# Kernel tuning notes

Measured on AMD Instinct MI355X. Metric: run time of the kernel, lower is better.

## Reference

```python
import jax, jax.numpy as jnp
import numpy as np

B, S, D = 4, 4096, 1024
H, DH = 16, 64            # heads, head dim (D = H*DH)
W = 256                   # local window size; S % W == 0
HID = 2 * D               # GEGLU hidden dim
LN_EPS = 1e-5


def setup_inputs() -> dict:
    key = jax.random.key(0)
    ks = jax.random.split(key, 8)
    w = lambda k, shp: (jax.random.normal(k, shp, jnp.float32) * 0.02)
    return {
        "x": jax.random.normal(ks[0], (B, S, D), jnp.float32),
        "ln1_g": jnp.ones((D,), jnp.float32), "ln1_b": jnp.zeros((D,), jnp.float32),
        "ln2_g": jnp.ones((D,), jnp.float32), "ln2_b": jnp.zeros((D,), jnp.float32),
        "Wq": w(ks[1], (D, D)), "Wk": w(ks[2], (D, D)), "Wv": w(ks[3], (D, D)),
        "Wo": w(ks[4], (D, D)), "bo": jnp.zeros((D,), jnp.float32),
        "W1": w(ks[5], (D, 2 * HID)), "b1": jnp.zeros((2 * HID,), jnp.float32),
        "W2": w(ks[6], (HID, D)), "b2": jnp.zeros((D,), jnp.float32),
    }


def layer_norm(x, g, b):
    mu = jnp.mean(x, axis=-1, keepdims=True)
    var = jnp.mean(jnp.square(x - mu), axis=-1, keepdims=True)
    return (x - mu) * jax.lax.rsqrt(var + LN_EPS) * g + b


def local_causal_attention(x, Wq, Wk, Wv, Wo, bo):
    b, s, d = x.shape
    nw = s // W
    def split_heads(t):  # [b,s,d] -> [b,H,nw,W,DH]
        return t.reshape(b, s, H, DH).transpose(0, 2, 1, 3).reshape(b, H, nw, W, DH)
    q = split_heads(x @ Wq)
    k = split_heads(x @ Wk)
    v = split_heads(x @ Wv)
    # look_backward=1: each window attends to [prev window, current window]
    def with_prev(t):  # [b,H,nw,W,DH] -> [b,H,nw,2W,DH]
        prev = jnp.pad(t, ((0, 0), (0, 0), (1, 0), (0, 0), (0, 0)))[:, :, :-1]
        return jnp.concatenate([prev, t], axis=3)
    kc, vc = with_prev(k), with_prev(v)
    scores = jnp.einsum("bhnqd,bhnkd->bhnqk", q, kc) * (DH ** -0.5)
    # positions: qpos = n*W + i ; kpos = (n-1)*W + j, j in [0,2W)
    n = jnp.arange(nw)[:, None, None]
    i = jnp.arange(W)[None, :, None]
    j = jnp.arange(2 * W)[None, None, :]
    qpos = n * W + i
    kpos = (n - 1) * W + j
    mask = (kpos <= qpos) & (kpos >= 0)  # causal + left-edge padding
    scores = jnp.where(mask[None, None], scores, jnp.finfo(scores.dtype).min)
    attn = jax.nn.softmax(scores, axis=-1)
    out = jnp.einsum("bhnqk,bhnkd->bhnqd", attn, vc)
    out = out.reshape(b, H, s, DH).transpose(0, 2, 1, 3).reshape(b, s, d)
    return out @ Wo + bo


def geglu(x, W1, b1, W2, b2):
    h = x @ W1 + b1
    a, g = jnp.split(h, 2, axis=-1)
    return (a * jax.nn.gelu(g, approximate=False)) @ W2 + b2


def reference(x, ln1_g, ln1_b, ln2_g, ln2_b, Wq, Wk, Wv, Wo, bo, W1, b1, W2, b2):
    x = x + local_causal_attention(layer_norm(x, ln1_g, ln1_b), Wq, Wk, Wv, Wo, bo)
    x = x + geglu(layer_norm(x, ln2_g, ln2_b), W1, b1, W2, b2)
    return x
```

## Files before the change

kernel.cpp:

```cpp
#include <hip/hip_runtime.h>
#include <hip/hip_bf16.h>

typedef __attribute__((ext_vector_type(4))) float f32x4;
typedef __attribute__((ext_vector_type(8))) short bf16x8;
typedef __attribute__((ext_vector_type(8))) unsigned short u16x8;

static __device__ __forceinline__ ushort f2b(float f) {
  union { float f; unsigned u; } v; v.f = f;
  unsigned r = v.u + 0x7fffu + ((v.u >> 16) & 1u);
  return (ushort)(r >> 16);
}

static __device__ __forceinline__ float gelu_fast(float g) {
  const float c0 = 0.7978845608028654f, c1 = 0.044715f;
  const float u = c0 * (g + c1 * g * g * g);
  const float e = __expf(2.0f * u);
  const float t = 1.0f - 2.0f / (e + 1.0f);
  return 0.5f * g * (1.0f + t);
}

static __device__ __forceinline__ void gload_lds16(const void* g, void* l) {
  __builtin_amdgcn_global_load_lds(
      (__attribute__((address_space(1))) void*)(g),
      (__attribute__((address_space(3))) void*)(l), 16, 0, 0);
}

__global__ __launch_bounds__(256) void transpose_cast_kernel(
    const float* __restrict__ W, ushort* __restrict__ Wt, int K, int N) {
  __shared__ float tile[32][33];
  const int n0 = blockIdx.x * 32, k0 = blockIdx.y * 32;
  const int tx = threadIdx.x, ty = threadIdx.y;
#pragma unroll
  for (int r = 0; r < 32; r += 8)
    tile[ty + r][tx] = W[(size_t)(k0 + ty + r) * N + n0 + tx];
  __syncthreads();
#pragma unroll
  for (int r = 0; r < 32; r += 8)
    Wt[(size_t)(n0 + ty + r) * K + k0 + tx] = f2b(tile[tx][ty + r]);
}

__global__ __launch_bounds__(256) void ln_kernel(
    const float* __restrict__ x, const float* __restrict__ g,
    const float* __restrict__ bb, ushort* __restrict__ out) {
  const int row = blockIdx.x;
  const float* xr = x + (size_t)row * 1024;
  const float4 v = *(const float4*)&xr[threadIdx.x * 4];
  float s = v.x + v.y + v.z + v.w;
  float s2 = v.x * v.x + v.y * v.y + v.z * v.z + v.w * v.w;
#pragma unroll
  for (int off = 32; off > 0; off >>= 1) {
    s += __shfl_down(s, off);
    s2 += __shfl_down(s2, off);
  }
  __shared__ float red[8];
  const int lane = threadIdx.x & 63, wv = threadIdx.x >> 6;
  if (lane == 0) { red[wv] = s; red[4 + wv] = s2; }
  __syncthreads();
  s = red[0] + red[1] + red[2] + red[3];
  s2 = red[4] + red[5] + red[6] + red[7];
  const float mu = s * (1.0f / 1024.0f);
  const float rs = rsqrtf(s2 * (1.0f / 1024.0f) - mu * mu + 1e-5f);
  const int c = threadIdx.x * 4;
  ushort4 o;
  o.x = f2b((v.x - mu) * rs * g[c + 0] + bb[c + 0]);
  o.y = f2b((v.y - mu) * rs * g[c + 1] + bb[c + 1]);
  o.z = f2b((v.z - mu) * rs * g[c + 2] + bb[c + 2]);
  o.w = f2b((v.w - mu) * rs * g[c + 3] + bb[c + 3]);
  *(ushort4*)&out[(size_t)row * 1024 + c] = o;
}

template <int MODE>
__global__ __launch_bounds__(512) void gemm256_kernel(
    const ushort* __restrict__ A, const ushort* __restrict__ Bt,
    const int M, const int N, const int K,
    ushort* __restrict__ Cb, float* __restrict__ Cf,
    const float* __restrict__ bias, const float* __restrict__ res) {
  __shared__ __align__(16) ushort lds[3 * 16384];

  const int ntn = N >> 8;
  const int bn = blockIdx.x % ntn;
  const int bm = blockIdx.x / ntn;
  const int tid = threadIdx.x;
  const int l = tid & 63, w = tid >> 6;
  const int wm = w >> 2, wn = w & 3;
  const int fr = l & 15, fq = l >> 4;

  const ushort* Ab = A + (size_t)bm * 256 * K;
  const ushort* Bb = Bt + (size_t)bn * 256 * K;

  const int srow = (l >> 2);
  const int scol = (((l & 3) ^ ((l >> 3) & 3)) * 8);

  f32x4 acc[8][4];
#pragma unroll
  for (int m = 0; m < 8; m++)
#pragma unroll
    for (int n = 0; n < 4; n++) acc[m][n] = (f32x4)0.0f;

  const int NT = K >> 5;

#define STAGE256(t)                                                            \
  {                                                                            \
    const int b3 = (t) % 3;                                                    \
    const size_t kk = (size_t)(t) * 32;                                        \
    _Pragma("unroll") for (int i = 0; i < 2; i++) {                            \
      const int r = (w * 2 + i) * 16 + srow;                                   \
      gload_lds16(Ab + (size_t)r * K + kk + scol,                              \
                  &lds[b3 * 16384 + (w * 2 + i) * 512]);                       \
      gload_lds16(Bb + (size_t)r * K + kk + scol,                              \
                  &lds[b3 * 16384 + 8192 + (w * 2 + i) * 512]);                \
    }                                                                          \
  }

  STAGE256(0);
  STAGE256(1);

  for (int t = 0; t < NT; ++t) {
    if (t + 2 < NT) {
      STAGE256(t + 2);
      asm volatile("s_waitcnt vmcnt(8)" ::: "memory");
    } else if (t + 1 < NT) {
      asm volatile("s_waitcnt vmcnt(4)" ::: "memory");
    } else {
      asm volatile("s_waitcnt vmcnt(0)" ::: "memory");
    }
    __builtin_amdgcn_s_barrier();
    asm volatile("" ::: "memory");

    const ushort* La = &lds[(t % 3) * 16384];
    const ushort* Lb = La + 8192;

    bf16x8 af[8], bf[4];
#pragma unroll
    for (int m = 0; m < 8; m++) {
      const int r = wm * 128 + m * 16 + fr;
      af[m] = *(const bf16x8*)&La[r * 32 + ((fq ^ ((r >> 1) & 3)) * 8)];
    }
#pragma unroll
    for (int n = 0; n < 4; n++) {
      const int r = wn * 64 + n * 16 + fr;
      bf[n] = *(const bf16x8*)&Lb[r * 32 + ((fq ^ ((r >> 1) & 3)) * 8)];
    }

    __builtin_amdgcn_s_setprio(1);
#pragma unroll
    for (int m = 0; m < 8; m++)
#pragma unroll
      for (int n = 0; n < 4; n++)
        acc[m][n] = __builtin_amdgcn_mfma_f32_16x16x32_bf16(af[m], bf[n], acc[m][n], 0, 0, 0);
    __builtin_amdgcn_s_setprio(0);

    asm volatile("" ::: "memory");
    __builtin_amdgcn_s_barrier();
  }
#undef STAGE256

  const int rowb = bm * 256 + wm * 128 + fq * 4;
  const int colb = bn * 256 + wn * 64 + fr;
#pragma unroll
  for (int m = 0; m < 8; m++) {
#pragma unroll
    for (int n = 0; n < 4; n++) {
      const int col = colb + n * 16;
#pragma unroll
      for (int j = 0; j < 4; j++) {
        const int row = rowb + m * 16 + j;
        float vv = acc[m][n][j];
        if (MODE == 0) {
          Cb[(size_t)row * N + col] = f2b(vv);
        } else if (MODE == 2) {
          if (col < 1024) vv *= 0.125f;
          Cb[(size_t)row * N + col] = f2b(vv);
        } else {
          Cf[(size_t)row * N + col] = vv + bias[col] + res[(size_t)row * N + col];
        }
      }
    }
  }
}

__global__ __launch_bounds__(512) void gemm_geglu_kernel(
    const ushort* __restrict__ A, const ushort* __restrict__ W1t,
    const float* __restrict__ b1, ushort* __restrict__ U) {
  const int K = 1024;
  __shared__ __align__(16) ushort lds[3 * 16384];

  const int bn = blockIdx.x & 15;
  const int bm = blockIdx.x >> 4;
  const int tid = threadIdx.x;
  const int l = tid & 63, w = tid >> 6;
  const int wm = w >> 2, wn = w & 3;
  const int fr = l & 15, fq = l >> 4;

  const ushort* Ab = A + (size_t)bm * 256 * K;
  const ushort* Bab = W1t + (size_t)bn * 128 * K;
  const ushort* Bgb = W1t + (size_t)(2048 + bn * 128) * K;

  const int srow = (l >> 2);
  const int scol = (((l & 3) ^ ((l >> 3) & 3)) * 8);
  const int brow = (tid >> 2);
  const int bscol = (((tid & 3) ^ ((tid >> 3) & 3)) * 8);

  f32x4 acca[8][2], accg[8][2];
#pragma unroll
  for (int m = 0; m < 8; m++)
#pragma unroll
    for (int n = 0; n < 2; n++) { acca[m][n] = (f32x4)0.0f; accg[m][n] = (f32x4)0.0f; }

  const int NT = K >> 5;

#define STAGEGL(t)                                                             \
  {                                                                            \
    const int b3 = (t) % 3;                                                    \
    const size_t kk = (size_t)(t) * 32;                                        \
    _Pragma("unroll") for (int i = 0; i < 2; i++) {                            \
      const int r = (w * 2 + i) * 16 + srow;                                   \
      gload_lds16(Ab + (size_t)r * K + kk + scol,                              \
                  &lds[b3 * 16384 + (w * 2 + i) * 512]);                       \
    }                                                                          \
    gload_lds16(Bab + (size_t)brow * K + kk + bscol,                           \
                &lds[b3 * 16384 + 8192 + w * 512]);                            \
    gload_lds16(Bgb + (size_t)brow * K + kk + bscol,                           \
                &lds[b3 * 16384 + 12288 + w * 512]);                           \
  }

  STAGEGL(0);
  STAGEGL(1);

  for (int t = 0; t < NT; ++t) {
    if (t + 2 < NT) {
      STAGEGL(t + 2);
      asm volatile("s_waitcnt vmcnt(8)" ::: "memory");
    } else if (t + 1 < NT) {
      asm volatile("s_waitcnt vmcnt(4)" ::: "memory");
    } else {
      asm volatile("s_waitcnt vmcnt(0)" ::: "memory");
    }
    __builtin_amdgcn_s_barrier();
    asm volatile("" ::: "memory");

    const ushort* La = &lds[(t % 3) * 16384];
    const ushort* Lba = La + 8192;
    const ushort* Lbg = La + 12288;

    bf16x8 af[8], ba[2], bg[2];
#pragma unroll
    for (int m = 0; m < 8; m++) {
      const int r = wm * 128 + m * 16 + fr;
      af[m] = *(const bf16x8*)&La[r * 32 + ((fq ^ ((r >> 1) & 3)) * 8)];
    }
#pragma unroll
    for (int n = 0; n < 2; n++) {
      const int r = wn * 32 + n * 16 + fr;
      ba[n] = *(const bf16x8*)&Lba[r * 32 + ((fq ^ ((r >> 1) & 3)) * 8)];
      bg[n] = *(const bf16x8*)&Lbg[r * 32 + ((fq ^ ((r >> 1) & 3)) * 8)];
    }

    __builtin_amdgcn_s_setprio(1);
#pragma unroll
    for (int m = 0; m < 8; m++)
#pragma unroll
      for (int n = 0; n < 2; n++) {
        acca[m][n] = __builtin_amdgcn_mfma_f32_16x16x32_bf16(af[m], ba[n], acca[m][n], 0, 0, 0);
        accg[m][n] = __builtin_amdgcn_mfma_f32_16x16x32_bf16(af[m], bg[n], accg[m][n], 0, 0, 0);
      }
    __builtin_amdgcn_s_setprio(0);

    asm volatile("" ::: "memory");
    __builtin_amdgcn_s_barrier();
  }
#undef STAGEGL

  const int rowb = bm * 256 + wm * 128 + fq * 4;
  const int colb = bn * 128 + wn * 32 + fr;
#pragma unroll
  for (int m = 0; m < 8; m++) {
#pragma unroll
    for (int n = 0; n < 2; n++) {
      const int col = colb + n * 16;
      const float b1a = b1[col];
      const float b1g = b1[2048 + col];
#pragma unroll
      for (int j = 0; j < 4; j++) {
        const int row = rowb + m * 16 + j;
        const float a = acca[m][n][j] + b1a;
        const float gg = accg[m][n][j] + b1g;
        U[(size_t)row * 2048 + col] = f2b(a * gelu_fast(gg));
      }
    }
  }
}

__global__ __launch_bounds__(256, 3) void attn_kernel(
    const ushort* __restrict__ Q, const ushort* __restrict__ Kb,
    const ushort* __restrict__ Vb, ushort* __restrict__ O, const int qs) {
  const int bx = blockIdx.x;
  const int n = bx & 15;
  const int h = (bx >> 4) & 15;
  const int b = bx >> 8;
  const int tid = threadIdx.x;
  const int lane = tid & 63, wv = tid >> 6;
  const int fr = lane & 15, fq = lane >> 4;

  __shared__ __align__(16) ushort Kl[64 * 72];
  __shared__ __align__(16) ushort Vt[64 * 70];
  __shared__ __align__(16) ushort Pl[4][64 * 68];

  const size_t qrow0 = (size_t)b * 4096 + (size_t)n * 256;

  bf16x8 qf[4][2];
#pragma unroll
  for (int m = 0; m < 4; m++)
#pragma unroll
    for (int kh = 0; kh < 2; kh++)
      qf[m][kh] = *(const bf16x8*)&Q[(qrow0 + wv * 64 + m * 16 + fr) * qs + h * 64 + kh * 32 + fq * 8];

  f32x4 oacc[4][4];
#pragma unroll
  for (int m = 0; m < 4; m++)
#pragma unroll
    for (int d = 0; d < 4; d++) oacc[m][d] = (f32x4)0.0f;

  float lsum[4][4];
#pragma unroll
  for (int m = 0; m < 4; m++)
#pragma unroll
    for (int j = 0; j < 4; j++) lsum[m][j] = 0.0f;

  const int c0 = (n == 0) ? 4 : 0;
  for (int c = c0; c < 8; c++) {
    const size_t kvrow0 =
        (size_t)((long long)b * 4096 + (long long)n * 256 + (long long)c * 64 - 256);
#pragma unroll
    for (int p = 0; p < 2; p++) {
      const int s = tid + p * 256;
      const int rr = s >> 3, cs2 = s & 7;
      *(u16x8*)&Kl[rr * 72 + cs2 * 8] =
          *(const u16x8*)&Kb[(kvrow0 + rr) * qs + h * 64 + cs2 * 8];
      const u16x8 vvv = *(const u16x8*)&Vb[(kvrow0 + rr) * qs + h * 64 + cs2 * 8];
#pragma unroll
      for (int i = 0; i < 8; i++) Vt[(cs2 * 8 + i) * 70 + rr] = vvv[i];
    }
    __syncthreads();

    if (c <= wv + 4) {
      const bool diag = (c == wv + 4);
#pragma unroll
      for (int nn = 0; nn < 4; nn++) {
        f32x4 sa[4];
#pragma unroll
        for (int m = 0; m < 4; m++) sa[m] = (f32x4)0.0f;
#pragma unroll
        for (int kh = 0; kh < 2; kh++) {
          const bf16x8 bk = *(const bf16x8*)&Kl[(nn * 16 + fr) * 72 + kh * 32 + fq * 8];
#pragma unroll
          for (int m = 0; m < 4; m++)
            sa[m] = __builtin_amdgcn_mfma_f32_16x16x32_bf16(qf[m][kh], bk, sa[m], 0, 0, 0);
        }
#pragma unroll
        for (int m = 0; m < 4; m++)
#pragma unroll
          for (int j = 0; j < 4; j++) {
            float p = __expf(sa[m][j]);
            if (diag && (nn * 16 + fr > m * 16 + fq * 4 + j)) p = 0.0f;
            lsum[m][j] += p;
            Pl[wv][(m * 16 + fq * 4 + j) * 68 + nn * 16 + fr] = f2b(p);
          }
      }
      __builtin_amdgcn_s_setprio(1);
#pragma unroll
      for (int kh = 0; kh < 2; kh++) {
        bf16x8 pa[4];
#pragma unroll
        for (int m = 0; m < 4; m++)
          pa[m] = *(const bf16x8*)&Pl[wv][(m * 16 + fr) * 68 + kh * 32 + fq * 8];
#pragma unroll
        for (int d = 0; d < 4; d++) {
          const bf16x8 vb = *(const bf16x8*)&Vt[(d * 16 + fr) * 70 + kh * 32 + fq * 8];
#pragma unroll
          for (int m = 0; m < 4; m++)
            oacc[m][d] = __builtin_amdgcn_mfma_f32_16x16x32_bf16(pa[m], vb, oacc[m][d], 0, 0, 0);
        }
      }
      __builtin_amdgcn_s_setprio(0);
    }
    __syncthreads();
  }

  float rl[4][4];
#pragma unroll
  for (int m = 0; m < 4; m++)
#pragma unroll
    for (int j = 0; j < 4; j++) {
      float t = lsum[m][j];
      t += __shfl_xor(t, 1);
      t += __shfl_xor(t, 2);
      t += __shfl_xor(t, 4);
      t += __shfl_xor(t, 8);
      rl[m][j] = 1.0f / t;
    }

#pragma unroll
  for (int m = 0; m < 4; m++)
#pragma unroll
    for (int d = 0; d < 4; d++)
#pragma unroll
      for (int j = 0; j < 4; j++) {
        const float o = oacc[m][d][j] * rl[m][j];
        O[(qrow0 + wv * 64 + m * 16 + fq * 4 + j) * 1024 + h * 64 + d * 16 + fr] = f2b(o);
      }
}

extern "C" void kernel_launch(void* const* d_in, const int* in_sizes, int n_in,
                              void* d_out, int out_size, void* d_ws, size_t ws_size,
                              hipStream_t stream) {
  (void)in_sizes; (void)n_in; (void)out_size; (void)ws_size;
  const float* x     = (const float*)d_in[0];
  const float* ln1_g = (const float*)d_in[1];
  const float* ln1_b = (const float*)d_in[2];
  const float* ln2_g = (const float*)d_in[3];
  const float* ln2_b = (const float*)d_in[4];
  const float* Wq    = (const float*)d_in[5];
  const float* Wk    = (const float*)d_in[6];
  const float* Wv    = (const float*)d_in[7];
  const float* Wo    = (const float*)d_in[8];
  const float* bo    = (const float*)d_in[9];
  const float* W1    = (const float*)d_in[10];
  const float* b1    = (const float*)d_in[11];
  const float* W2    = (const float*)d_in[12];
  const float* b2    = (const float*)d_in[13];

  char* ws = (char*)d_ws;
  const size_t MB = 1ull << 20;
  ushort* WQKVT = (ushort*)(ws + 0 * MB);
  ushort* WOT = (ushort*)(ws + 6 * MB);
  ushort* W1T = (ushort*)(ws + 8 * MB);
  ushort* W2T = (ushort*)(ws + 16 * MB);
  ushort* LN1 = (ushort*)(ws + 20 * MB);
  ushort* ATT = LN1;
  ushort* QKV = (ushort*)(ws + 52 * MB);
  ushort* LN2 = (ushort*)(ws + 52 * MB);
  ushort* U   = (ushort*)(ws + 84 * MB);
  float*  X1  = (float*)d_out;
  float*  OUT = (float*)d_out;

  const dim3 tb(32, 8);
  transpose_cast_kernel<<<dim3(32, 32), tb, 0, stream>>>(Wq, WQKVT, 1024, 1024);
  transpose_cast_kernel<<<dim3(32, 32), tb, 0, stream>>>(Wk, WQKVT + (size_t)1024 * 1024, 1024, 1024);
  transpose_cast_kernel<<<dim3(32, 32), tb, 0, stream>>>(Wv, WQKVT + (size_t)2048 * 1024, 1024, 1024);
  transpose_cast_kernel<<<dim3(32, 32), tb, 0, stream>>>(Wo, WOT, 1024, 1024);
  transpose_cast_kernel<<<dim3(128, 32), tb, 0, stream>>>(W1, W1T, 1024, 4096);
  transpose_cast_kernel<<<dim3(32, 64), tb, 0, stream>>>(W2, W2T, 2048, 1024);

  ln_kernel<<<16384, 256, 0, stream>>>(x, ln1_g, ln1_b, LN1);

  gemm256_kernel<2><<<64 * 12, 512, 0, stream>>>(LN1, WQKVT, 16384, 3072, 1024,
                                                 QKV, nullptr, nullptr, nullptr);

  attn_kernel<<<1024, 256, 0, stream>>>(QKV, QKV + 1024, QKV + 2048, ATT, 3072);

  gemm256_kernel<1><<<64 * 4, 512, 0, stream>>>(ATT, WOT, 16384, 1024, 1024,
                                                nullptr, X1, bo, x);

  ln_kernel<<<16384, 256, 0, stream>>>(X1, ln2_g, ln2_b, LN2);

  gemm_geglu_kernel<<<64 * 16, 512, 0, stream>>>(LN2, W1T, b1, U);

  gemm256_kernel<1><<<64 * 4, 512, 0, stream>>>(U, W2T, 16384, 1024, 2048,
                                                nullptr, OUT, b2, X1);
}
```

Baseline: 557.0 us.

## Restructure GEMM mainloops to BK=64 double-buffered, four-phase interleaved loads

Both the 256x256 GEMM and the fused GEGLU GEMM move from a triple-buffered BK=32 pipeline to a double-buffered BK=64 pipeline with an 8-way XOR swizzle. Each K-step is split into four quarter-tile MFMA phases, and the next tile's global-to-LDS loads are spread across those phases. The aim is to halve loop iterations and barrier overhead per K and to overlap loads with compute at finer grain. In exchange there are more barriers per iteration, only one tile of prefetch depth, and LDS grows to 128KB, which limits occupancy.

```diff
diff --git a/kernel.cpp b/kernel.cpp
--- a/kernel.cpp
+++ b/kernel.cpp
@@ -24,6 +24,8 @@
       (__attribute__((address_space(1))) void*)(g),
       (__attribute__((address_space(3))) void*)(l), 16, 0, 0);
 }
+
+#define MFMA_BF16 __builtin_amdgcn_mfma_f32_16x16x32_bf16
 
 __global__ __launch_bounds__(256) void transpose_cast_kernel(
     const float* __restrict__ W, ushort* __restrict__ Wt, int K, int N) {
@@ -75,7 +77,7 @@
     const int M, const int N, const int K,
     ushort* __restrict__ Cb, float* __restrict__ Cf,
     const float* __restrict__ bias, const float* __restrict__ res) {
-  __shared__ __align__(16) ushort lds[3 * 16384];
+  __shared__ __align__(16) ushort lds[2 * 32768];
 
   const int ntn = N >> 8;
   const int bn = blockIdx.x % ntn;
@@ -88,8 +90,8 @@
   const ushort* Ab = A + (size_t)bm * 256 * K;
   const ushort* Bb = Bt + (size_t)bn * 256 * K;
 
-  const int srow = (l >> 2);
-  const int scol = (((l & 3) ^ ((l >> 3) & 3)) * 8);
+  const int lr = l >> 3;
+  const int sc = (((l & 7) ^ lr) * 8);
 
   f32x4 acc[8][4];
 #pragma unroll
@@ -97,63 +99,121 @@
 #pragma unroll
     for (int n = 0; n < 4; n++) acc[m][n] = (f32x4)0.0f;
 
-  const int NT = K >> 5;
-
-#define STAGE256(t)                                                            \
-  {                                                                            \
-    const int b3 = (t) % 3;                                                    \
-    const size_t kk = (size_t)(t) * 32;                                        \
-    _Pragma("unroll") for (int i = 0; i < 2; i++) {                            \
-      const int r = (w * 2 + i) * 16 + srow;                                   \
-      gload_lds16(Ab + (size_t)r * K + kk + scol,                              \
-                  &lds[b3 * 16384 + (w * 2 + i) * 512]);                       \
-      gload_lds16(Bb + (size_t)r * K + kk + scol,                              \
-                  &lds[b3 * 16384 + 8192 + (w * 2 + i) * 512]);                \
-    }                                                                          \
-  }
-
-  STAGE256(0);
-  STAGE256(1);
+  const int NT = K >> 6;
+
+#define STG_A(h, tt)                                                           \
+  { _Pragma("unroll") for (int i = 0; i < 2; i++) {                            \
+      const int rr = (h) * 128 + i * 64 + w * 8;                               \
+      gload_lds16(Ab + (size_t)(rr + lr) * K + (size_t)(tt) * 64 + sc,         \
+                  &lds[((tt) & 1) * 32768 + rr * 64]); } }
+#define STG_B(h, tt)                                                           \
+  { _Pragma("unroll") for (int i = 0; i < 2; i++) {                            \
+      const int rr = (h) * 128 + i * 64 + w * 8;                               \
+      gload_lds16(Bb + (size_t)(rr + lr) * K + (size_t)(tt) * 64 + sc,         \
+                  &lds[((tt) & 1) * 32768 + 16384 + rr * 64]); } }
+
+  STG_A(0, 0); STG_A(1, 0); STG_B(0, 0); STG_B(1, 0);
 
   for (int t = 0; t < NT; ++t) {
-    if (t + 2 < NT) {
-      STAGE256(t + 2);
-      asm volatile("s_waitcnt vmcnt(8)" ::: "memory");
-    } else if (t + 1 < NT) {
-      asm volatile("s_waitcnt vmcnt(4)" ::: "memory");
+    const ushort* La = &lds[(t & 1) * 32768];
+    const ushort* Lb = La + 16384;
+    bf16x8 af[4][2], bf[4][2];
+
+    if (t + 1 < NT) {
+      STG_A(0, t + 1);
+      asm volatile("s_waitcnt vmcnt(2)" ::: "memory");
     } else {
       asm volatile("s_waitcnt vmcnt(0)" ::: "memory");
     }
     __builtin_amdgcn_s_barrier();
     asm volatile("" ::: "memory");
-
-    const ushort* La = &lds[(t % 3) * 16384];
-    const ushort* Lb = La + 8192;
-
-    bf16x8 af[8], bf[4];
-#pragma unroll
-    for (int m = 0; m < 8; m++) {
+#pragma unroll
+    for (int m = 0; m < 4; m++) {
       const int r = wm * 128 + m * 16 + fr;
-      af[m] = *(const bf16x8*)&La[r * 32 + ((fq ^ ((r >> 1) & 3)) * 8)];
-    }
-#pragma unroll
-    for (int n = 0; n < 4; n++) {
+#pragma unroll
+      for (int kk = 0; kk < 2; kk++)
+        af[m][kk] = *(const bf16x8*)&La[r * 64 + (((kk * 4 + fq) ^ (r & 7)) * 8)];
+    }
+#pragma unroll
+    for (int n = 0; n < 2; n++) {
       const int r = wn * 64 + n * 16 + fr;
-      bf[n] = *(const bf16x8*)&Lb[r * 32 + ((fq ^ ((r >> 1) & 3)) * 8)];
-    }
-
-    __builtin_amdgcn_s_setprio(1);
-#pragma unroll
-    for (int m = 0; m < 8; m++)
-#pragma unroll
-      for (int n = 0; n < 4; n++)
-        acc[m][n] = __builtin_amdgcn_mfma_f32_16x16x32_bf16(af[m], bf[n], acc[m][n], 0, 0, 0);
-    __builtin_amdgcn_s_setprio(0);
-
+#pragma unroll
+      for (int kk = 0; kk < 2; kk++)
+        bf[n][kk] = *(const bf16x8*)&Lb[r * 64 + (((kk * 4 + fq) ^ (r & 7)) * 8)];
+    }
+    __builtin_amdgcn_s_setprio(1);
+#pragma unroll
+    for (int m = 0; m < 4; m++)
+#pragma unroll
+      for (int n = 0; n < 2; n++)
+#pragma unroll
+        for (int kk = 0; kk < 2; kk++)
+          acc[m][n] = MFMA_BF16(af[m][kk], bf[n][kk], acc[m][n], 0, 0, 0);
+    __builtin_amdgcn_s_setprio(0);
+    asm volatile("" ::: "memory");
+    __builtin_amdgcn_s_barrier();
+
+    if (t + 1 < NT) STG_A(1, t + 1);
+#pragma unroll
+    for (int n = 2; n < 4; n++) {
+      const int r = wn * 64 + n * 16 + fr;
+#pragma unroll
+      for (int kk = 0; kk < 2; kk++)
+        bf[n][kk] = *(const bf16x8*)&Lb[r * 64 + (((kk * 4 + fq) ^ (r & 7)) * 8)];
+    }
+    __builtin_amdgcn_s_barrier();
+    asm volatile("" ::: "memory");
+    __builtin_amdgcn_s_setprio(1);
+#pragma unroll
+    for (int m = 0; m < 4; m++)
+#pragma unroll
+      for (int n = 2; n < 4; n++)
+#pragma unroll
+        for (int kk = 0; kk < 2; kk++)
+          acc[m][n] = MFMA_BF16(af[m][kk], bf[n][kk], acc[m][n], 0, 0, 0);
+    __builtin_amdgcn_s_setprio(0);
+    asm volatile("" ::: "memory");
+    __builtin_amdgcn_s_barrier();
+
+    if (t + 1 < NT) STG_B(0, t + 1);
+#pragma unroll
+    for (int m = 0; m < 4; m++) {
+      const int r = wm * 128 + (m + 4) * 16 + fr;
+#pragma unroll
+      for (int kk = 0; kk < 2; kk++)
+        af[m][kk] = *(const bf16x8*)&La[r * 64 + (((kk * 4 + fq) ^ (r & 7)) * 8)];
+    }
+    __builtin_amdgcn_s_barrier();
+    asm volatile("" ::: "memory");
+    __builtin_amdgcn_s_setprio(1);
+#pragma unroll
+    for (int m = 0; m < 4; m++)
+#pragma unroll
+      for (int n = 0; n < 2; n++)
+#pragma unroll
+        for (int kk = 0; kk < 2; kk++)
+          acc[m + 4][n] = MFMA_BF16(af[m][kk], bf[n][kk], acc[m + 4][n], 0, 0, 0);
+    __builtin_amdgcn_s_setprio(0);
+    asm volatile("" ::: "memory");
+    __builtin_amdgcn_s_barrier();
+
+    if (t + 1 < NT) STG_B(1, t + 1);
+    __builtin_amdgcn_s_barrier();
+    asm volatile("" ::: "memory");
+    __builtin_amdgcn_s_setprio(1);
+#pragma unroll
+    for (int m = 0; m < 4; m++)
+#pragma unroll
+      for (int n = 2; n < 4; n++)
+#pragma unroll
+        for (int kk = 0; kk < 2; kk++)
+          acc[m + 4][n] = MFMA_BF16(af[m][kk], bf[n][kk], acc[m + 4][n], 0, 0, 0);
+    __builtin_amdgcn_s_setprio(0);
     asm volatile("" ::: "memory");
     __builtin_amdgcn_s_barrier();
   }
-#undef STAGE256
+#undef STG_A
+#undef STG_B
 
   const int rowb = bm * 256 + wm * 128 + fq * 4;
   const int colb = bn * 256 + wn * 64 + fr;
@@ -183,7 +243,7 @@
     const ushort* __restrict__ A, const ushort* __restrict__ W1t,
     const float* __restrict__ b1, ushort* __restrict__ U) {
   const int K = 1024;
-  __shared__ __align__(16) ushort lds[3 * 16384];
+  __shared__ __align__(16) ushort lds[2 * 32768];
 
   const int bn = blockIdx.x & 15;
   const int bm = blockIdx.x >> 4;
@@ -196,10 +256,8 @@
   const ushort* Bab = W1t + (size_t)bn * 128 * K;
   const ushort* Bgb = W1t + (size_t)(2048 + bn * 128) * K;
 
-  const int srow = (l >> 2);
-  const int scol = (((l & 3) ^ ((l >> 3) & 3)) * 8);
-  const int brow = (tid >> 2);
-  const int bscol = (((tid & 3) ^ ((tid >> 3) & 3)) * 8);
+  const int lr = l >> 3;
+  const int sc = (((l & 7) ^ lr) * 8);
 
   f32x4 acca[8][2], accg[8][2];
 #pragma unroll
@@ -207,69 +265,128 @@
 #pragma unroll
     for (int n = 0; n < 2; n++) { acca[m][n] = (f32x4)0.0f; accg[m][n] = (f32x4)0.0f; }
 
-  const int NT = K >> 5;
-
-#define STAGEGL(t)                                                             \
-  {                                                                            \
-    const int b3 = (t) % 3;                                                    \
-    const size_t kk = (size_t)(t) * 32;                                        \
-    _Pragma("unroll") for (int i = 0; i < 2; i++) {                            \
-      const int r = (w * 2 + i) * 16 + srow;                                   \
-      gload_lds16(Ab + (size_t)r * K + kk + scol,                              \
-                  &lds[b3 * 16384 + (w * 2 + i) * 512]);                       \
-    }                                                                          \
-    gload_lds16(Bab + (size_t)brow * K + kk + bscol,                           \
-                &lds[b3 * 16384 + 8192 + w * 512]);                            \
-    gload_lds16(Bgb + (size_t)brow * K + kk + bscol,                           \
-                &lds[b3 * 16384 + 12288 + w * 512]);                           \
-  }
-
-  STAGEGL(0);
-  STAGEGL(1);
+  const int NT = K >> 6;
+
+#define STG_GA(h, tt)                                                          \
+  { _Pragma("unroll") for (int i = 0; i < 2; i++) {                            \
+      const int rr = (h) * 128 + i * 64 + w * 8;                               \
+      gload_lds16(Ab + (size_t)(rr + lr) * K + (size_t)(tt) * 64 + sc,         \
+                  &lds[((tt) & 1) * 32768 + rr * 64]); } }
+#define STG_BA(tt)                                                             \
+  { _Pragma("unroll") for (int i = 0; i < 2; i++) {                            \
+      const int rr = i * 64 + w * 8;                                           \
+      gload_lds16(Bab + (size_t)(rr + lr) * K + (size_t)(tt) * 64 + sc,        \
+                  &lds[((tt) & 1) * 32768 + 16384 + rr * 64]); } }
+#define STG_BG(tt)                                                             \
+  { _Pragma("unroll") for (int i = 0; i < 2; i++) {                            \
+      const int rr = i * 64 + w * 8;                                           \
+      gload_lds16(Bgb + (size_t)(rr + lr) * K + (size_t)(tt) * 64 + sc,        \
+                  &lds[((tt) & 1) * 32768 + 24576 + rr * 64]); } }
+
+  STG_GA(0, 0); STG_GA(1, 0); STG_BA(0); STG_BG(0);
 
   for (int t = 0; t < NT; ++t) {
-    if (t + 2 < NT) {
-      STAGEGL(t + 2);
-      asm volatile("s_waitcnt vmcnt(8)" ::: "memory");
-    } else if (t + 1 < NT) {
-      asm volatile("s_waitcnt vmcnt(4)" ::: "memory");
+    const ushort* La = &lds[(t & 1) * 32768];
+    const ushort* Lba = La + 16384;
+    const ushort* Lbg = La + 24576;
+    bf16x8 af[4][2], ba[2][2], bg[2][2];
+
+    if (t + 1 < NT) {
+      STG_GA(0, t + 1);
+      asm volatile("s_waitcnt vmcnt(2)" ::: "memory");
     } else {
       asm volatile("s_waitcnt vmcnt(0)" ::: "memory");
     }
     __builtin_amdgcn_s_barrier();
     asm volatile("" ::: "memory");
-
-    const ushort* La = &lds[(t % 3) * 16384];
-    const ushort* Lba = La + 8192;
-    const ushort* Lbg = La + 12288;
-
-    bf16x8 af[8], ba[2], bg[2];
-#pragma unroll
-    for (int m = 0; m < 8; m++) {
+#pragma unroll
+    for (int m = 0; m < 4; m++) {
       const int r = wm * 128 + m * 16 + fr;
-      af[m] = *(const bf16x8*)&La[r * 32 + ((fq ^ ((r >> 1) & 3)) * 8)];
+#pragma unroll
+      for (int kk = 0; kk < 2; kk++)
+        af[m][kk] = *(const bf16x8*)&La[r * 64 + (((kk * 4 + fq) ^ (r & 7)) * 8)];
     }
 #pragma unroll
     for (int n = 0; n < 2; n++) {
       const int r = wn * 32 + n * 16 + fr;
-      ba[n] = *(const bf16x8*)&Lba[r * 32 + ((fq ^ ((r >> 1) & 3)) * 8)];
-      bg[n] = *(const bf16x8*)&Lbg[r * 32 + ((fq ^ ((r >> 1) & 3)) * 8)];
-    }
-
-    __builtin_amdgcn_s_setprio(1);
-#pragma unroll
-    for (int m = 0; m < 8; m++)
-#pragma unroll
-      for (int n = 0; n < 2; n++) {
-        acca[m][n] = __builtin_amdgcn_mfma_f32_16x16x32_bf16(af[m], ba[n], acca[m][n], 0, 0, 0);
-        accg[m][n] = __builtin_amdgcn_mfma_f32_16x16x32_bf16(af[m], bg[n], accg[m][n], 0, 0, 0);
-      }
-    __builtin_amdgcn_s_setprio(0);
-
+#pragma unroll
+      for (int kk = 0; kk < 2; kk++)
+        ba[n][kk] = *(const bf16x8*)&Lba[r * 64 + (((kk * 4 + fq) ^ (r & 7)) * 8)];
+    }
+    __builtin_amdgcn_s_setprio(1);
+#pragma unroll
+    for (int m = 0; m < 4; m++)
+#pragma unroll
+      for (int n = 0; n < 2; n++)
+#pragma unroll
+        for (int kk = 0; kk < 2; kk++)
+          acca[m][n] = MFMA_BF16(af[m][kk], ba[n][kk], acca[m][n], 0, 0, 0);
+    __builtin_amdgcn_s_setprio(0);
+    asm volatile("" ::: "memory");
+    __builtin_amdgcn_s_barrier();
+
+    if (t + 1 < NT) STG_GA(1, t + 1);
+#pragma unroll
+    for (int n = 0; n < 2; n++) {
+      const int r = wn * 32 + n * 16 + fr;
+#pragma unroll
+      for (int kk = 0; kk < 2; kk++)
+        bg[n][kk] = *(const bf16x8*)&Lbg[r * 64 + (((kk * 4 + fq) ^ (r & 7)) * 8)];
+    }
+    __builtin_amdgcn_s_barrier();
+    asm volatile("" ::: "memory");
+    __builtin_amdgcn_s_setprio(1);
+#pragma unroll
+    for (int m = 0; m < 4; m++)
+#pragma unroll
+      for (int n = 0; n < 2; n++)
+#pragma unroll
+        for (int kk = 0; kk < 2; kk++)
+          accg[m][n] = MFMA_BF16(af[m][kk], bg[n][kk], accg[m][n], 0, 0, 0);
+    __builtin_amdgcn_s_setprio(0);
+    asm volatile("" ::: "memory");
+    __builtin_amdgcn_s_barrier();
+
+    if (t + 1 < NT) STG_BA(t + 1);
+#pragma unroll
+    for (int m = 0; m < 4; m++) {
+      const int r = wm * 128 + (m + 4) * 16 + fr;
+#pragma unroll
+      for (int kk = 0; kk < 2; kk++)
+        af[m][kk] = *(const bf16x8*)&La[r * 64 + (((kk * 4 + fq) ^ (r & 7)) * 8)];
+    }
+    __builtin_amdgcn_s_barrier();
+    asm volatile("" ::: "memory");
+    __builtin_amdgcn_s_setprio(1);
+#pragma unroll
+    for (int m = 0; m < 4; m++)
+#pragma unroll
+      for (int n = 0; n < 2; n++)
+#pragma unroll
+        for (int kk = 0; kk < 2; kk++)
+          acca[m + 4][n] = MFMA_BF16(af[m][kk], ba[n][kk], acca[m + 4][n], 0, 0, 0);
+    __builtin_amdgcn_s_setprio(0);
+    asm volatile("" ::: "memory");
+    __builtin_amdgcn_s_barrier();
+
+    if (t + 1 < NT) STG_BG(t + 1);
+    __builtin_amdgcn_s_barrier();
+    asm volatile("" ::: "memory");
+    __builtin_amdgcn_s_setprio(1);
+#pragma unroll
+    for (int m = 0; m < 4; m++)
+#pragma unroll
+      for (int n = 0; n < 2; n++)
+#pragma unroll
+        for (int kk = 0; kk < 2; kk++)
+          accg[m + 4][n] = MFMA_BF16(af[m][kk], bg[n][kk], accg[m + 4][n], 0, 0, 0);
+    __builtin_amdgcn_s_setprio(0);
     asm volatile("" ::: "memory");
     __builtin_amdgcn_s_barrier();
   }
-#undef STAGEGL
+#undef STG_GA
+#undef STG_BA
+#undef STG_BG
 
   const int rowb = bm * 256 + wm * 128 + fq * 4;
   const int colb = bn * 128 + wn * 32 + fr;
@@ -355,7 +472,7 @@
           const bf16x8 bk = *(const bf16x8*)&Kl[(nn * 16 + fr) * 72 + kh * 32 + fq * 8];
 #pragma unroll
           for (int m = 0; m < 4; m++)
-            sa[m] = __builtin_amdgcn_mfma_f32_16x16x32_bf16(qf[m][kh], bk, sa[m], 0, 0, 0);
+            sa[m] = MFMA_BF16(qf[m][kh], bk, sa[m], 0, 0, 0);
         }
 #pragma unroll
         for (int m = 0; m < 4; m++)
@@ -379,7 +496,7 @@
           const bf16x8 vb = *(const bf16x8*)&Vt[(d * 16 + fr) * 70 + kh * 32 + fq * 8];
 #pragma unroll
           for (int m = 0; m < 4; m++)
-            oacc[m][d] = __builtin_amdgcn_mfma_f32_16x16x32_bf16(pa[m], vb, oacc[m][d], 0, 0, 0);
+            oacc[m][d] = MFMA_BF16(pa[m], vb, oacc[m][d], 0, 0, 0);
         }
       }
       __builtin_amdgcn_s_setprio(0);
```

New measurement: 535.7 us. 3.8% less time.

## Restructure GEMM mainloops into K=64 double-buffered four-phase schedule with interleaved loads

Applied to the files above, without the earlier changes.

Both the generic 256x256 GEMM and the fused GEGLU GEMM move from a triple-buffered K=32 pipeline to a double-buffered K=64 tile. Each tile is split into four compute phases, and the next tile's global->LDS loads are issued in pieces between phases. The LDS layout gains a wider 8-way XOR swizzle, and launch bounds now request two blocks per CU. The goal is fewer barriers per unit of work and better overlap of loads with MFMA, at the cost of more barriers inside each tile and tighter register and LDS pressure.

```diff
diff --git a/kernel.cpp b/kernel.cpp
--- a/kernel.cpp
+++ b/kernel.cpp
@@ -24,6 +24,8 @@
       (__attribute__((address_space(1))) void*)(g),
       (__attribute__((address_space(3))) void*)(l), 16, 0, 0);
 }
+
+#define MFMA_BF16 __builtin_amdgcn_mfma_f32_16x16x32_bf16
 
 __global__ __launch_bounds__(256) void transpose_cast_kernel(
     const float* __restrict__ W, ushort* __restrict__ Wt, int K, int N) {
@@ -70,12 +72,12 @@
 }
 
 template <int MODE>
-__global__ __launch_bounds__(512) void gemm256_kernel(
+__global__ __launch_bounds__(512, 2) void gemm256_kernel(
     const ushort* __restrict__ A, const ushort* __restrict__ Bt,
     const int M, const int N, const int K,
     ushort* __restrict__ Cb, float* __restrict__ Cf,
     const float* __restrict__ bias, const float* __restrict__ res) {
-  __shared__ __align__(16) ushort lds[3 * 16384];
+  __shared__ __align__(16) ushort lds[2 * 32768];
 
   const int ntn = N >> 8;
   const int bn = blockIdx.x % ntn;
@@ -88,8 +90,19 @@
   const ushort* Ab = A + (size_t)bm * 256 * K;
   const ushort* Bb = Bt + (size_t)bn * 256 * K;
 
-  const int srow = (l >> 2);
-  const int scol = (((l & 3) ^ ((l >> 3) & 3)) * 8);
+  const int lr = l >> 3;
+  const int sc = (((l & 7) ^ lr) * 8);
+
+  const char* ldsc = (const char*)lds;
+  const int fr7 = fr & 7;
+  const unsigned s0 = (unsigned)((fq ^ fr7) * 16);
+  const unsigned s1 = (unsigned)(((4 + fq) ^ fr7) * 16);
+  const unsigned cA0 = (unsigned)((wm * 128 + fr) * 128) + s0;
+  const unsigned cA1 = (unsigned)((wm * 128 + fr) * 128) + s1;
+  const unsigned cB0 = 32768u + (unsigned)((wn * 64 + fr) * 128) + s0;
+  const unsigned cB1 = 32768u + (unsigned)((wn * 64 + fr) * 128) + s1;
+  const unsigned dA0 = cA0 + 65536u, dA1 = cA1 + 65536u;
+  const unsigned dB0 = cB0 + 65536u, dB1 = cB1 + 65536u;
 
   f32x4 acc[8][4];
 #pragma unroll
@@ -97,63 +110,102 @@
 #pragma unroll
     for (int n = 0; n < 4; n++) acc[m][n] = (f32x4)0.0f;
 
-  const int NT = K >> 5;
-
-#define STAGE256(t)                                                            \
+  const int NT = K >> 6;
+
+#define STG_A(h, tt, DSTU)                                                     \
+  { _Pragma("unroll") for (int i = 0; i < 2; i++) {                            \
+      const int rr = (h) * 128 + i * 64 + w * 8;                               \
+      gload_lds16(Ab + (size_t)(rr + lr) * K + (size_t)(tt) * 64 + sc,         \
+                  &lds[(DSTU) + rr * 64]); } }
+#define STG_B(h, tt, DSTU)                                                     \
+  { _Pragma("unroll") for (int i = 0; i < 2; i++) {                            \
+      const int rr = (h) * 128 + i * 64 + w * 8;                               \
+      gload_lds16(Bb + (size_t)(rr + lr) * K + (size_t)(tt) * 64 + sc,         \
+                  &lds[(DSTU) + 16384 + rr * 64]); } }
+
+#define GPHASES(tt, bA0v, bA1v, bB0v, bB1v, DSTU, HASNEXT)                     \
   {                                                                            \
-    const int b3 = (t) % 3;                                                    \
-    const size_t kk = (size_t)(t) * 32;                                        \
-    _Pragma("unroll") for (int i = 0; i < 2; i++) {                            \
-      const int r = (w * 2 + i) * 16 + srow;                                   \
-      gload_lds16(Ab + (size_t)r * K + kk + scol,                              \
-                  &lds[b3 * 16384 + (w * 2 + i) * 512]);                       \
-      gload_lds16(Bb + (size_t)r * K + kk + scol,                              \
-                  &lds[b3 * 16384 + 8192 + (w * 2 + i) * 512]);                \
-    }                                                                          \
-  }
-
-  STAGE256(0);
-  STAGE256(1);
-
-  for (int t = 0; t < NT; ++t) {
-    if (t + 2 < NT) {
-      STAGE256(t + 2);
-      asm volatile("s_waitcnt vmcnt(8)" ::: "memory");
-    } else if (t + 1 < NT) {
-      asm volatile("s_waitcnt vmcnt(4)" ::: "memory");
-    } else {
-      asm volatile("s_waitcnt vmcnt(0)" ::: "memory");
-    }
-    __builtin_amdgcn_s_barrier();
-    asm volatile("" ::: "memory");
-
-    const ushort* La = &lds[(t % 3) * 16384];
-    const ushort* Lb = La + 8192;
-
-    bf16x8 af[8], bf[4];
-#pragma unroll
-    for (int m = 0; m < 8; m++) {
-      const int r = wm * 128 + m * 16 + fr;
-      af[m] = *(const bf16x8*)&La[r * 32 + ((fq ^ ((r >> 1) & 3)) * 8)];
-    }
-#pragma unroll
-    for (int n = 0; n < 4; n++) {
-      const int r = wn * 64 + n * 16 + fr;
-      bf[n] = *(const bf16x8*)&Lb[r * 32 + ((fq ^ ((r >> 1) & 3)) * 8)];
-    }
-
-    __builtin_amdgcn_s_setprio(1);
-#pragma unroll
-    for (int m = 0; m < 8; m++)
-#pragma unroll
-      for (int n = 0; n < 4; n++)
-        acc[m][n] = __builtin_amdgcn_mfma_f32_16x16x32_bf16(af[m], bf[n], acc[m][n], 0, 0, 0);
-    __builtin_amdgcn_s_setprio(0);
-
-    asm volatile("" ::: "memory");
-    __builtin_amdgcn_s_barrier();
-  }
-#undef STAGE256
+    bf16x8 af[4][2], bfv[4][2];                                                \
+                                  \
+    if (HASNEXT) {                                                             \
+      STG_A(0, (tt) + 1, DSTU);                                                \
+      asm volatile("s_waitcnt vmcnt(2)" ::: "memory");                         \
+    } else {                                                                   \
+      asm volatile("s_waitcnt vmcnt(0)" ::: "memory");                         \
+    }                                                                          \
+    __builtin_amdgcn_s_barrier();                                              \
+    asm volatile("" ::: "memory");                                             \
+    _Pragma("unroll") for (int m = 0; m < 4; m++) {                            \
+      af[m][0] = *(const bf16x8*)(ldsc + (bA0v) + m * 2048);                   \
+      af[m][1] = *(const bf16x8*)(ldsc + (bA1v) + m * 2048);                   \
+    }                                                                          \
+    _Pragma("unroll") for (int n = 0; n < 2; n++) {                            \
+      bfv[n][0] = *(const bf16x8*)(ldsc + (bB0v) + n * 2048);                  \
+      bfv[n][1] = *(const bf16x8*)(ldsc + (bB1v) + n * 2048);                  \
+    }                                                                          \
+    __builtin_amdgcn_s_setprio(1);                                             \
+    _Pragma("unroll") for (int m = 0; m < 4; m++)                              \
+      _Pragma("unroll") for (int n = 0; n < 2; n++)                            \
+        _Pragma("unroll") for (int kk = 0; kk < 2; kk++)                       \
+          acc[m][n] = MFMA_BF16(af[m][kk], bfv[n][kk], acc[m][n], 0, 0, 0);    \
+    __builtin_amdgcn_s_setprio(0);                                             \
+    asm volatile("" ::: "memory");                                             \
+    __builtin_amdgcn_s_barrier();                                              \
+                                                \
+    if (HASNEXT) STG_A(1, (tt) + 1, DSTU);                                     \
+    _Pragma("unroll") for (int n = 2; n < 4; n++) {                            \
+      bfv[n][0] = *(const bf16x8*)(ldsc + (bB0v) + n * 2048);                  \
+      bfv[n][1] = *(const bf16x8*)(ldsc + (bB1v) + n * 2048);                  \
+    }                                                                          \
+    __builtin_amdgcn_s_barrier();                                              \
+    asm volatile("" ::: "memory");                                             \
+    __builtin_amdgcn_s_setprio(1);                                             \
+    _Pragma("unroll") for (int m = 0; m < 4; m++)                              \
+      _Pragma("unroll") for (int n = 2; n < 4; n++)                            \
+        _Pragma("unroll") for (int kk = 0; kk < 2; kk++)                       \
+          acc[m][n] = MFMA_BF16(af[m][kk], bfv[n][kk], acc[m][n], 0, 0, 0);    \
+    __builtin_amdgcn_s_setprio(0);                                             \
+    asm volatile("" ::: "memory");                                             \
+    __builtin_amdgcn_s_barrier();                                              \
+                                                \
+    if (HASNEXT) STG_B(0, (tt) + 1, DSTU);                                     \
+    _Pragma("unroll") for (int m = 0; m < 4; m++) {                            \
+      af[m][0] = *(const bf16x8*)(ldsc + (bA0v) + (m + 4) * 2048);             \
+      af[m][1] = *(const bf16x8*)(ldsc + (bA1v) + (m + 4) * 2048);             \
+    }                                                                          \
+    __builtin_amdgcn_s_barrier();                                              \
+    asm volatile("" ::: "memory");                                             \
+    __builtin_amdgcn_s_setprio(1);                                             \
+    _Pragma("unroll") for (int m = 0; m < 4; m++)                              \
+      _Pragma("unroll") for (int n = 0; n < 2; n++)                            \
+        _Pragma("unroll") for (int kk = 0; kk < 2; kk++)                       \
+          acc[m + 4][n] = MFMA_BF16(af[m][kk], bfv[n][kk], acc[m + 4][n], 0, 0, 0); \
+    __builtin_amdgcn_s_setprio(0);                                             \
+    asm volatile("" ::: "memory");                                             \
+    __builtin_amdgcn_s_barrier();                                              \
+                                                \
+    if (HASNEXT) STG_B(1, (tt) + 1, DSTU);                                     \
+    __builtin_amdgcn_s_barrier();                                              \
+    asm volatile("" ::: "memory");                                             \
+    __builtin_amdgcn_s_setprio(1);                                             \
+    _Pragma("unroll") for (int m = 0; m < 4; m++)                              \
+      _Pragma("unroll") for (int n = 2; n < 4; n++)                            \
+        _Pragma("unroll") for (int kk = 0; kk < 2; kk++)                       \
+          acc[m + 4][n] = MFMA_BF16(af[m][kk], bfv[n][kk], acc[m + 4][n], 0, 0, 0); \
+    __builtin_amdgcn_s_setprio(0);                                             \
+    asm volatile("" ::: "memory");                                             \
+    __builtin_amdgcn_s_barrier();                                              \
+  }
+
+  STG_A(0, 0, 0); STG_A(1, 0, 0); STG_B(0, 0, 0); STG_B(1, 0, 0);
+
+  for (int t = 0; t < NT; t += 2) {
+    GPHASES(t, cA0, cA1, cB0, cB1, 32768, true);
+    GPHASES(t + 1, dA0, dA1, dB0, dB1, 0, (t + 2 < NT));
+  }
+#undef GPHASES
+#undef STG_A
+#undef STG_B
 
   const int rowb = bm * 256 + wm * 128 + fq * 4;
   const int colb = bn * 256 + wn * 64 + fr;
@@ -179,11 +231,11 @@
   }
 }
 
-__global__ __launch_bounds__(512) void gemm_geglu_kernel(
+__global__ __launch_bounds__(512, 2) void gemm_geglu_kernel(
     const ushort* __restrict__ A, const ushort* __restrict__ W1t,
     const float* __restrict__ b1, ushort* __restrict__ U) {
   const int K = 1024;
-  __shared__ __align__(16) ushort lds[3 * 16384];
+  __shared__ __align__(16) ushort lds[2 * 32768];
 
   const int bn = blockIdx.x & 15;
   const int bm = blockIdx.x >> 4;
@@ -196,10 +248,19 @@
   const ushort* Bab = W1t + (size_t)bn * 128 * K;
   const ushort* Bgb = W1t + (size_t)(2048 + bn * 128) * K;
 
-  const int srow = (l >> 2);
-  const int scol = (((l & 3) ^ ((l >> 3) & 3)) * 8);
-  const int brow = (tid >> 2);
-  const int bscol = (((tid & 3) ^ ((tid >> 3) & 3)) * 8);
+  const int lr = l >> 3;
+  const int sc = (((l & 7) ^ lr) * 8);
+
+  const char* ldsc = (const char*)lds;
+  const int fr7 = fr & 7;
+  const unsigned s0 = (unsigned)((fq ^ fr7) * 16);
+  const unsigned s1 = (unsigned)(((4 + fq) ^ fr7) * 16);
+  const unsigned cA0 = (unsigned)((wm * 128 + fr) * 128) + s0;
+  const unsigned cA1 = (unsigned)((wm * 128 + fr) * 128) + s1;
+  const unsigned cBa0 = 32768u + (unsigned)((wn * 32 + fr) * 128) + s0;
+  const unsigned cBa1 = 32768u + (unsigned)((wn * 32 + fr) * 128) + s1;
+  const unsigned dA0 = cA0 + 65536u, dA1 = cA1 + 65536u;
+  const unsigned dBa0 = cBa0 + 65536u, dBa1 = cBa1 + 65536u;
 
   f32x4 acca[8][2], accg[8][2];
 #pragma unroll
@@ -207,69 +268,108 @@
 #pragma unroll
     for (int n = 0; n < 2; n++) { acca[m][n] = (f32x4)0.0f; accg[m][n] = (f32x4)0.0f; }
 
-  const int NT = K >> 5;
-
-#define STAGEGL(t)                                                             \
+  const int NT = K >> 6;
+
+#define STG_GA(h, tt, DSTU)                                                    \
+  { _Pragma("unroll") for (int i = 0; i < 2; i++) {                            \
+      const int rr = (h) * 128 + i * 64 + w * 8;                               \
+      gload_lds16(Ab + (size_t)(rr + lr) * K + (size_t)(tt) * 64 + sc,         \
+                  &lds[(DSTU) + rr * 64]); } }
+#define STG_BA(tt, DSTU)                                                       \
+  { _Pragma("unroll") for (int i = 0; i < 2; i++) {                            \
+      const int rr = i * 64 + w * 8;                                           \
+      gload_lds16(Bab + (size_t)(rr + lr) * K + (size_t)(tt) * 64 + sc,        \
+                  &lds[(DSTU) + 16384 + rr * 64]); } }
+#define STG_BG(tt, DSTU)                                                       \
+  { _Pragma("unroll") for (int i = 0; i < 2; i++) {                            \
+      const int rr = i * 64 + w * 8;                                           \
+      gload_lds16(Bgb + (size_t)(rr + lr) * K + (size_t)(tt) * 64 + sc,        \
+                  &lds[(DSTU) + 24576 + rr * 64]); } }
+
+#define GLPHASES(tt, bA0v, bA1v, bBa0v, bBa1v, DSTU, HASNEXT)                  \
   {                                                                            \
-    const int b3 = (t) % 3;                                                    \
-    const size_t kk = (size_t)(t) * 32;                                        \
-    _Pragma("unroll") for (int i = 0; i < 2; i++) {                            \
-      const int r = (w * 2 + i) * 16 + srow;                                   \
-      gload_lds16(Ab + (size_t)r * K + kk + scol,                              \
-                  &lds[b3 * 16384 + (w * 2 + i) * 512]);                       \
-    }                                                                          \
-    gload_lds16(Bab + (size_t)brow * K + kk + bscol,                           \
-                &lds[b3 * 16384 + 8192 + w * 512]);                            \
-    gload_lds16(Bgb + (size_t)brow * K + kk + bscol,                           \
-                &lds[b3 * 16384 + 12288 + w * 512]);                           \
-  }
-
-  STAGEGL(0);
-  STAGEGL(1);
-
-  for (int t = 0; t < NT; ++t) {
-    if (t + 2 < NT) {
-      STAGEGL(t + 2);
-      asm volatile("s_waitcnt vmcnt(8)" ::: "memory");
-    } else if (t + 1 < NT) {
-      asm volatile("s_waitcnt vmcnt(4)" ::: "memory");
-    } else {
-      asm volatile("s_waitcnt vmcnt(0)" ::: "memory");
-    }
-    __builtin_amdgcn_s_barrier();
-    asm volatile("" ::: "memory");
-
-    const ushort* La = &lds[(t % 3) * 16384];
-    const ushort* Lba = La + 8192;
-    const ushort* Lbg = La + 12288;
-
-    bf16x8 af[8], ba[2], bg[2];
-#pragma unroll
-    for (int m = 0; m < 8; m++) {
-      const int r = wm * 128 + m * 16 + fr;
-      af[m] = *(const bf16x8*)&La[r * 32 + ((fq ^ ((r >> 1) & 3)) * 8)];
-    }
-#pragma unroll
-    for (int n = 0; n < 2; n++) {
-      const int r = wn * 32 + n * 16 + fr;
-      ba[n] = *(const bf16x8*)&Lba[r * 32 + ((fq ^ ((r >> 1) & 3)) * 8)];
-      bg[n] = *(const bf16x8*)&Lbg[r * 32 + ((fq ^ ((r >> 1) & 3)) * 8)];
-    }
-
-    __builtin_amdgcn_s_setprio(1);
-#pragma unroll
-    for (int m = 0; m < 8; m++)
-#pragma unroll
-      for (int n = 0; n < 2; n++) {
-        acca[m][n] = __builtin_amdgcn_mfma_f32_16x16x32_bf16(af[m], ba[n], acca[m][n], 0, 0, 0);
-        accg[m][n] = __builtin_amdgcn_mfma_f32_16x16x32_bf16(af[m], bg[n], accg[m][n], 0, 0, 0);
-      }
-    __builtin_amdgcn_s_setprio(0);
-
-    asm volatile("" ::: "memory");
-    __builtin_amdgcn_s_barrier();
-  }
-#undef STAGEGL
+    bf16x8 af[4][2], ba[2][2], bg[2][2];                                       \
+                                            \
+    if (HASNEXT) {                                                             \
+      STG_GA(0, (tt) + 1, DSTU);                                               \
+      asm volatile("s_waitcnt vmcnt(2)" ::: "memory");                         \
+    } else {                                                                   \
+      asm volatile("s_waitcnt vmcnt(0)" ::: "memory");                         \
+    }                                                                          \
+    __builtin_amdgcn_s_barrier();                                              \
+    asm volatile("" ::: "memory");                                             \
+    _Pragma("unroll") for (int m = 0; m < 4; m++) {                            \
+      af[m][0] = *(const bf16x8*)(ldsc + (bA0v) + m * 2048);                   \
+      af[m][1] = *(const bf16x8*)(ldsc + (bA1v) + m * 2048);                   \
+    }                                                                          \
+    _Pragma("unroll") for (int n = 0; n < 2; n++) {                            \
+      ba[n][0] = *(const bf16x8*)(ldsc + (bBa0v) + n * 2048);                  \
+      ba[n][1] = *(const bf16x8*)(ldsc + (bBa1v) + n * 2048);                  \
+    }                                                                          \
+    __builtin_amdgcn_s_setprio(1);                                             \
+    _Pragma("unroll") for (int m = 0; m < 4; m++)                              \
+      _Pragma("unroll") for (int n = 0; n < 2; n++)                            \
+        _Pragma("unroll") for (int kk = 0; kk < 2; kk++)                       \
+          acca[m][n] = MFMA_BF16(af[m][kk], ba[n][kk], acca[m][n], 0, 0, 0);   \
+    __builtin_amdgcn_s_setprio(0);                                             \
+    asm volatile("" ::: "memory");                                             \
+    __builtin_amdgcn_s_barrier();                                              \
+                                                     \
+    if (HASNEXT) STG_GA(1, (tt) + 1, DSTU);                                    \
+    _Pragma("unroll") for (int n = 0; n < 2; n++) {                            \
+      bg[n][0] = *(const bf16x8*)(ldsc + (bBa0v) + 16384 + n * 2048);          \
+      bg[n][1] = *(const bf16x8*)(ldsc + (bBa1v) + 16384 + n * 2048);          \
+    }                                                                          \
+    __builtin_amdgcn_s_barrier();                                              \
+    asm volatile("" ::: "memory");                                             \
+    __builtin_amdgcn_s_setprio(1);                                             \
+    _Pragma("unroll") for (int m = 0; m < 4; m++)                              \
+      _Pragma("unroll") for (int n = 0; n < 2; n++)                            \
+        _Pragma("unroll") for (int kk = 0; kk < 2; kk++)                       \
+          accg[m][n] = MFMA_BF16(af[m][kk], bg[n][kk], accg[m][n], 0, 0, 0);   \
+    __builtin_amdgcn_s_setprio(0);                                             \
+    asm volatile("" ::: "memory");                                             \
+    __builtin_amdgcn_s_barrier();                                              \
+                                                     \
+    if (HASNEXT) STG_BA((tt) + 1, DSTU);                                       \
+    _Pragma("unroll") for (int m = 0; m < 4; m++) {                            \
+      af[m][0] = *(const bf16x8*)(ldsc + (bA0v) + (m + 4) * 2048);             \
+      af[m][1] = *(const bf16x8*)(ldsc + (bA1v) + (m + 4) * 2048);             \
+    }                                                                          \
+    __builtin_amdgcn_s_barrier();                                              \
+    asm volatile("" ::: "memory");                                             \
+    __builtin_amdgcn_s_setprio(1);                                             \
+    _Pragma("unroll") for (int m = 0; m < 4; m++)                              \
+      _Pragma("unroll") for (int n = 0; n < 2; n++)                            \
+        _Pragma("unroll") for (int kk = 0; kk < 2; kk++)                       \
+          acca[m + 4][n] = MFMA_BF16(af[m][kk], ba[n][kk], acca[m + 4][n], 0, 0, 0); \
+    __builtin_amdgcn_s_setprio(0);                                             \
+    asm volatile("" ::: "memory");                                             \
+    __builtin_amdgcn_s_barrier();                                              \
+                                                     \
+    if (HASNEXT) STG_BG((tt) + 1, DSTU);                                       \
+    __builtin_amdgcn_s_barrier();                                              \
+    asm volatile("" ::: "memory");                                             \
+    __builtin_amdgcn_s_setprio(1);                                             \
+    _Pragma("unroll") for (int m = 0; m < 4; m++)                              \
+      _Pragma("unroll") for (int n = 0; n < 2; n++)                            \
+        _Pragma("unroll") for (int kk = 0; kk < 2; kk++)                       \
+          accg[m + 4][n] = MFMA_BF16(af[m][kk], bg[n][kk], accg[m + 4][n], 0, 0, 0); \
+    __builtin_amdgcn_s_setprio(0);                                             \
+    asm volatile("" ::: "memory");                                             \
+    __builtin_amdgcn_s_barrier();                                              \
+  }
+
+  STG_GA(0, 0, 0); STG_GA(1, 0, 0); STG_BA(0, 0); STG_BG(0, 0);
+
+  for (int t = 0; t < NT; t += 2) {
+    GLPHASES(t, cA0, cA1, cBa0, cBa1, 32768, true);
+    GLPHASES(t + 1, dA0, dA1, dBa0, dBa1, 0, (t + 2 < NT));
+  }
+#undef GLPHASES
+#undef STG_GA
+#undef STG_BA
+#undef STG_BG
 
   const int rowb = bm * 256 + wm * 128 + fq * 4;
   const int colb = bn * 128 + wn * 32 + fr;
@@ -355,7 +455,7 @@
           const bf16x8 bk = *(const bf16x8*)&Kl[(nn * 16 + fr) * 72 + kh * 32 + fq * 8];
 #pragma unroll
           for (int m = 0; m < 4; m++)
-            sa[m] = __builtin_amdgcn_mfma_f32_16x16x32_bf16(qf[m][kh], bk, sa[m], 0, 0, 0);
+            sa[m] = MFMA_BF16(qf[m][kh], bk, sa[m], 0, 0, 0);
         }
 #pragma unroll
         for (int m = 0; m < 4; m++)
@@ -379,7 +479,7 @@
           const bf16x8 vb = *(const bf16x8*)&Vt[(d * 16 + fr) * 70 + kh * 32 + fq * 8];
 #pragma unroll
           for (int m = 0; m < 4; m++)
-            oacc[m][d] = __builtin_amdgcn_mfma_f32_16x16x32_bf16(pa[m], vb, oacc[m][d], 0, 0, 0);
+            oacc[m][d] = MFMA_BF16(pa[m], vb, oacc[m][d], 0, 0, 0);
         }
       }
       __builtin_amdgcn_s_setprio(0);
```

Measured after the change: 528.3 us. -5.1%, faster.
